# Performance work log

Hardware: AMD Instinct MI355X
Metric: run time of the kernel (lower is better)

Reference implementation:

```python
import jax, jax.numpy as jnp
import numpy as np

B, S, D, H, OUT = 64, 512, 128, 2, 8
TD, VD, AD = 300, 35, 74
DH = D // H
EPS = 1e-5


def _layernorm(x, g, b):
    m = jnp.mean(x, -1, keepdims=True)
    v = jnp.var(x, -1, keepdims=True)
    return (x - m) * jax.lax.rsqrt(v + EPS) * g + b


def _attn_neg(q_in, k_in, v_in, Wq, bq, Wk, bk, Wv, bv, Wd, bd, g, beta):
    # MultiheadAttention2: probs = 1 - softmax(scores). dropout off (eval).
    b_, s_, _ = q_in.shape
    q = (q_in @ Wq + bq).reshape(b_, s_, H, DH).transpose(0, 2, 1, 3)
    k = (k_in @ Wk + bk).reshape(b_, k_in.shape[1], H, DH).transpose(0, 2, 1, 3)
    v = (v_in @ Wv + bv).reshape(b_, v_in.shape[1], H, DH).transpose(0, 2, 1, 3)
    scores = jnp.einsum('bhqd,bhkd->bhqk', q, k) / jnp.sqrt(jnp.float32(DH))
    probs = 1.0 - jax.nn.softmax(scores, axis=-1)
    ctx = jnp.einsum('bhqk,bhkd->bhqd', probs, v)
    ctx = ctx.transpose(0, 2, 1, 3).reshape(b_, s_, D)
    return _layernorm(ctx @ Wd + bd, g, beta)


def _gru_dir(x, Wih, Whh, bih, bhh):
    # torch GRU, gate order (r, z, n). x: [B,S,D] -> [B,S,H=128]
    gx = x @ Wih.T + bih  # [B,S,3H]
    gx_t = gx.transpose(1, 0, 2)  # [S,B,3H]

    def step(h, g_t):
        gh = h @ Whh.T + bhh
        xr, xz, xn = jnp.split(g_t, 3, -1)
        hr, hz, hn = jnp.split(gh, 3, -1)
        r = jax.nn.sigmoid(xr + hr)
        z = jax.nn.sigmoid(xz + hz)
        n = jnp.tanh(xn + r * hn)
        h_new = (1.0 - z) * n + z * h
        return h_new, h_new

    h0 = jnp.zeros((x.shape[0], D), x.dtype)
    _, hs = jax.lax.scan(step, h0, gx_t)
    return hs.transpose(1, 0, 2)


def _bigru(x, Wih, Whh, bih, bhh):
    fwd = _gru_dir(x, Wih[0], Whh[0], bih[0], bhh[0])
    bwd = _gru_dir(x[:, ::-1], Wih[1], Whh[1], bih[1], bhh[1])[:, ::-1]
    return jnp.concatenate([fwd, bwd], -1)


def setup_inputs() -> dict:
    key = jax.random.key(0)
    ks = iter(jax.random.split(key, 40))
    sc = 0.05

    def rn(shape, s=sc):
        return jax.random.normal(next(ks), shape, jnp.float32) * s

    inp = {
        'text_features': rn((B, S, TD), 1.0),
        'visual_features': rn((B, S, VD), 1.0),
        'audio_features': rn((B, S, AD), 1.0),
        'fc1W': rn((TD, D)), 'fc1b': rn((D,)),
        'fc2W': rn((VD, D)), 'fc2b': rn((D,)),
        'fc3W': rn((AD, D)), 'fc3b': rn((D,)),
        # 6 attention units: [ta_a, ta_b, tv_a, tv_b, va_a, va_b]
        'Wq': rn((6, D, D)), 'bq': rn((6, D)),
        'Wk': rn((6, D, D)), 'bk': rn((6, D)),
        'Wv': rn((6, D, D)), 'bv': rn((6, D)),
        'Wd': rn((6, D, D)), 'bd': rn((6, D)),
        'ln_g': jnp.ones((6, D), jnp.float32), 'ln_b': jnp.zeros((6, D), jnp.float32),
        # 3 bidirectional GRUs: [gru1(text), gru2(visual), gru3(audio)] x [fwd, bwd]
        'gWih': rn((3, 2, 3 * D, D)), 'gWhh': rn((3, 2, 3 * D, D)),
        'gbih': rn((3, 2, 3 * D)), 'gbhh': rn((3, 2, 3 * D)),
        # head: Linear(3D,2D) -> BN(eval) -> ReLU6 -> Linear(2D,out)
        'fW1': rn((3 * D, 2 * D)), 'fb1': rn((2 * D,)),
        'bn_g': jnp.ones((2 * D,), jnp.float32), 'bn_b': jnp.zeros((2 * D,), jnp.float32),
        'fW2': rn((2 * D, OUT)), 'fb2': rn((OUT,)),
    }
    return inp


def reference(text_features, visual_features, audio_features,
              fc1W, fc1b, fc2W, fc2b, fc3W, fc3b,
              Wq, bq, Wk, bk, Wv, bv, Wd, bd, ln_g, ln_b,
              gWih, gWhh, gbih, gbhh,
              fW1, fb1, bn_g, bn_b, fW2, fb2):
    t = text_features @ fc1W + fc1b
    v = visual_features @ fc2W + fc2b
    a = audio_features @ fc3W + fc3b

    def A(i, q, k, val):
        return _attn_neg(q, k, val, Wq[i], bq[i], Wk[i], bk[i], Wv[i], bv[i],
                         Wd[i], bd[i], ln_g[i], ln_b[i])

    # CrossAttention(a,b): b_out = a_attn(a,b,b); a_out = b_attn(b,a,a)
    audio_out1 = A(0, t, a, a)   # text_audio.a_attention
    text_out1 = A(1, a, t, t)    # text_audio.b_attention
    visual_out1 = A(2, t, v, v)  # text_visual.a_attention
    text_out2 = A(3, v, t, t)    # text_visual.b_attention
    audio_out2 = A(4, v, a, a)   # visual_audio.a_attention
    visual_out2 = A(5, a, v, v)  # visual_audio.b_attention

    text_out = (text_out1 + text_out2) / 2
    visual_out = (visual_out1 + visual_out2) / 2
    audio_out = (audio_out1 + audio_out2) / 2

    text_out = _bigru(text_out, gWih[0], gWhh[0], gbih[0], gbhh[0])
    visual_out = _bigru(visual_out, gWih[1], gWhh[1], gbih[1], gbhh[1])
    audio_out = _bigru(audio_out, gWih[2], gWhh[2], gbih[2], gbhh[2])

    out = jnp.concatenate([text_out, visual_out, audio_out], -1)  # [B,S,6D]
    out = jnp.mean((out[:, :, 3 * D:] + out[:, :, :3 * D]) / 2, axis=1)  # [B,3D]

    h = out @ fW1 + fb1
    # BatchNorm1d in eval with running stats (mean=0, var=1)
    h = h * jax.lax.rsqrt(jnp.float32(1.0 + EPS)) * bn_g + bn_b
    h = jnp.clip(h, 0.0, 6.0)  # ReLU6
    return h @ fW2 + fb2
```

## Files before the change

### kernel.cpp

```cpp
#include <hip/hip_runtime.h>
#include <hip/hip_bf16.h>

#define BB 64
#define SS 512
#define DD 128
#define NROW (BB * SS)
#define SZ ((size_t)NROW * DD)

#define LOG2E 1.4426950408889634f
#define QSCALE (0.125f * LOG2E)

typedef __attribute__((ext_vector_type(8))) short short8;
typedef __attribute__((ext_vector_type(4))) float f32x4;

#define WB_P1 0
#define WB_P2 40960
#define WB_P3 49152
#define WB_QKVD 61440
#define WB_WIH 454656
#define WB_WHH 749568
#define WB_TOTAL 1044480

__device__ __forceinline__ float frcp_(float x) { return __builtin_amdgcn_rcpf(x); }
__device__ __forceinline__ float fexp2_(float x) { return __builtin_amdgcn_exp2f(x); }
__device__ __forceinline__ float b2f(unsigned short u) {
  union { unsigned int i; float f; } x; x.i = ((unsigned int)u) << 16; return x.f;
}
__device__ __forceinline__ unsigned short f2b(float f) {
  __hip_bfloat16 b = __float2bfloat16(f);
  return *reinterpret_cast<unsigned short*>(&b);
}
__device__ __forceinline__ unsigned short f2b_trunc(float f) {
  union { float f; unsigned int i; } x; x.f = f; return (unsigned short)(x.i >> 16);
}

__global__ __launch_bounds__(256) void prep_kernel(
    const float* __restrict__ fc1W, const float* __restrict__ fc2W,
    const float* __restrict__ fc3W, const float* __restrict__ Wq,
    const float* __restrict__ Wk, const float* __restrict__ Wv,
    const float* __restrict__ Wd, const float* __restrict__ gWih,
    const float* __restrict__ gWhh, const float* __restrict__ gbih,
    const float* __restrict__ gbhh, const float* __restrict__ bq,
    unsigned short* __restrict__ WB, float* __restrict__ gbihs,
    float* __restrict__ bqs) {
  for (int idx = blockIdx.x * 256 + threadIdx.x; idx < WB_TOTAL;
       idx += gridDim.x * 256) {
    float v;
    if (idx < WB_P2) {
      int n = idx / 320, k = idx % 320;
      v = (k < 300) ? fc1W[k * 128 + n] : 0.f;
    } else if (idx < WB_P3) {
      int r = idx - WB_P2; int n = r >> 6, k = r & 63;
      v = (k < 35) ? fc2W[k * 128 + n] : 0.f;
    } else if (idx < WB_QKVD) {
      int r = idx - WB_P3; int n = r / 96, k = r % 96;
      v = (k < 74) ? fc3W[k * 128 + n] : 0.f;
    } else if (idx < WB_WIH) {
      int r = idx - WB_QKVD;
      int op = r / 98304; int r2 = r % 98304;
      int u = r2 >> 14; int r3 = r2 & 16383;
      int n = r3 >> 7, k = r3 & 127;
      const float* src = (op == 0) ? Wq : (op == 1) ? Wk : (op == 2) ? Wv : Wd;
      v = src[u * 16384 + k * 128 + n];
      if (op == 0) v *= QSCALE;
    } else if (idx < WB_WHH) {
      int r = idx - WB_WIH;
      int r3 = r % 49152;
      int gate = (r3 >> 7) >> 7;
      v = gWih[r] * (gate < 2 ? LOG2E : 2.f * LOG2E);
    } else {
      int r = idx - WB_WHH;
      int r3 = r % 49152;
      int gate = (r3 >> 7) >> 7;
      v = gWhh[r] * (gate < 2 ? LOG2E : 2.f * LOG2E);
    }
    WB[idx] = f2b(v);
  }
  for (int idx = blockIdx.x * 256 + threadIdx.x; idx < 6 * 384;
       idx += gridDim.x * 256) {
    int gate = (idx % 384) >> 7;
    float v = gbih[idx] + (gate < 2 ? gbhh[idx] : 0.f);
    gbihs[idx] = v * (gate < 2 ? LOG2E : 2.f * LOG2E);
  }
  for (int idx = blockIdx.x * 256 + threadIdx.x; idx < 6 * 128;
       idx += gridDim.x * 256) {
    bqs[idx] = bq[idx] * QSCALE;
  }
}

struct GArg {
  const void* A; const unsigned short* W; const float* bias; void* C;
  int Ka, Kp, abf, cbf, cs; float* vsum;
};
struct GArgs { GArg g[18]; };

__global__ __launch_bounds__(256) void gemm_b(GArgs args) {
  const GArg ga = args.g[blockIdx.z];
  const int ny = blockIdx.y;
  __shared__ unsigned short As[128 * 40];
  __shared__ unsigned short Ws[128 * 40];
  const int t = threadIdx.x;
  const int w = t >> 6, lane = t & 63, q = lane >> 4, lm = lane & 15;
  const int wm = w >> 1, wn = w & 1;
  const int m0 = blockIdx.x * 128;
  const int row = t >> 1, cb = (t & 1) * 16;
  f32x4 acc[4][4];
#pragma unroll
  for (int i = 0; i < 4; ++i)
#pragma unroll
    for (int j = 0; j < 4; ++j) acc[i][j] = (f32x4){0.f, 0.f, 0.f, 0.f};

  for (int kt = 0; kt < ga.Kp; kt += 32) {
    {
      const float* Ag = (const float*)ga.A + (size_t)(m0 + row) * ga.Ka + kt + cb;
      unsigned short tmp[16];
#pragma unroll
      for (int j = 0; j < 16; ++j) {
        int k = kt + cb + j;
        tmp[j] = (k < ga.Ka) ? f2b(Ag[j]) : 0;
      }
      *reinterpret_cast<short8*>(&As[row * 40 + cb]) =
          *reinterpret_cast<short8*>(&tmp[0]);
      *reinterpret_cast<short8*>(&As[row * 40 + cb + 8]) =
          *reinterpret_cast<short8*>(&tmp[8]);
    }
    {
      const unsigned short* Wg =
          ga.W + (size_t)(ny * 128 + row) * ga.Kp + kt + cb;
      short8 v0 = *reinterpret_cast<const short8*>(Wg);
      short8 v1 = *reinterpret_cast<const short8*>(Wg + 8);
      *reinterpret_cast<short8*>(&Ws[row * 40 + cb]) = v0;
      *reinterpret_cast<short8*>(&Ws[row * 40 + cb + 8]) = v1;
    }
    __syncthreads();
    short8 af[4], bfv[4];
#pragma unroll
    for (int mi = 0; mi < 4; ++mi)
      af[mi] = *reinterpret_cast<const short8*>(
          &As[(wm * 64 + mi * 16 + lm) * 40 + q * 8]);
#pragma unroll
    for (int ni = 0; ni < 4; ++ni)
      bfv[ni] = *reinterpret_cast<const short8*>(
          &Ws[(wn * 64 + ni * 16 + lm) * 40 + q * 8]);
#pragma unroll
    for (int mi = 0; mi < 4; ++mi)
#pragma unroll
      for (int ni = 0; ni < 4; ++ni)
        acc[mi][ni] = __builtin_amdgcn_mfma_f32_16x16x32_bf16(
            af[mi], bfv[ni], acc[mi][ni], 0, 0, 0);
    __syncthreads();
  }
#pragma unroll
  for (int ni = 0; ni < 4; ++ni) {
    const int colg = ny * 128 + wn * 64 + ni * 16 + lm;
    const float bv = ga.bias[colg];
#pragma unroll
    for (int mi = 0; mi < 4; ++mi) {
      const int rg = m0 + wm * 64 + mi * 16 + q * 4;
#pragma unroll
      for (int r = 0; r < 4; ++r) {
        float v = acc[mi][ni][r] + bv;
        if (ga.cbf)
          ((unsigned short*)ga.C)[(size_t)(rg + r) * ga.cs + colg] = f2b(v);
        else
          ((float*)ga.C)[(size_t)(rg + r) * ga.cs + colg] = v;
      }
    }
  }
  if (ga.vsum) {
    float* vp = ga.vsum + (size_t)(m0 >> 9) * 128;
#pragma unroll
    for (int ni = 0; ni < 4; ++ni) {
      const int colg = wn * 64 + ni * 16 + lm;
      float s = 16.f * ga.bias[colg];
#pragma unroll
      for (int mi = 0; mi < 4; ++mi)
#pragma unroll
        for (int r = 0; r < 4; ++r) s += acc[mi][ni][r];
      atomicAdd(&vp[colg], s);
    }
  }
}

#define CST 5120

__global__ __launch_bounds__(256) void gemm_k128(GArgs args) {
  const GArg ga = args.g[blockIdx.z];
  const int ny = blockIdx.y;
  __shared__ unsigned short As4[4 * CST];
  __shared__ unsigned short Ws4[4 * CST];
  const int t = threadIdx.x;
  const int w = t >> 6, lane = t & 63, q = lane >> 4, lm = lane & 15;
  const int wm = w >> 1, wn = w & 1;
  const int m0 = blockIdx.x * 128;

  const int srow = t >> 4, scol = (t & 15) * 8;
  const int sc = scol >> 5, soff = scol & 31;
  {
    const unsigned short* Ab =
        (const unsigned short*)ga.A + (size_t)(m0 + srow) * 128 + scol;
    const unsigned short* Wg =
        ga.W + (size_t)(ny * 128 + srow) * 128 + scol;
#pragma unroll
    for (int p = 0; p < 8; ++p) {
      short8 av = *reinterpret_cast<const short8*>(Ab + (size_t)p * 16 * 128);
      short8 wv = *reinterpret_cast<const short8*>(Wg + (size_t)p * 16 * 128);
      *reinterpret_cast<short8*>(&As4[sc * CST + (srow + p * 16) * 40 + soff]) = av;
      *reinterpret_cast<short8*>(&Ws4[sc * CST + (srow + p * 16) * 40 + soff]) = wv;
    }
  }
  __syncthreads();

  f32x4 acc[4][4];
#pragma unroll
  for (int i = 0; i < 4; ++i)
#pragma unroll
    for (int j = 0; j < 4; ++j) acc[i][j] = (f32x4){0.f, 0.f, 0.f, 0.f};

#pragma unroll
  for (int c = 0; c < 4; ++c) {
    short8 af[4], bfv[4];
#pragma unroll
    for (int mi = 0; mi < 4; ++mi)
      af[mi] = *reinterpret_cast<const short8*>(
          &As4[c * CST + (wm * 64 + mi * 16 + lm) * 40 + q * 8]);
#pragma unroll
    for (int ni = 0; ni < 4; ++ni)
      bfv[ni] = *reinterpret_cast<const short8*>(
          &Ws4[c * CST + (wn * 64 + ni * 16 + lm) * 40 + q * 8]);
#pragma unroll
    for (int mi = 0; mi < 4; ++mi)
#pragma unroll
      for (int ni = 0; ni < 4; ++ni)
        acc[mi][ni] = __builtin_amdgcn_mfma_f32_16x16x32_bf16(
            af[mi], bfv[ni], acc[mi][ni], 0, 0, 0);
  }

#pragma unroll
  for (int ni = 0; ni < 4; ++ni) {
    const int colg = ny * 128 + wn * 64 + ni * 16 + lm;
    const float bv = ga.bias[colg];
#pragma unroll
    for (int mi = 0; mi < 4; ++mi) {
      const int rg = m0 + wm * 64 + mi * 16 + q * 4;
#pragma unroll
      for (int r = 0; r < 4; ++r) {
        float v = acc[mi][ni][r] + bv;
        if (ga.cbf)
          ((unsigned short*)ga.C)[(size_t)(rg + r) * ga.cs + colg] = f2b(v);
        else
          ((float*)ga.C)[(size_t)(rg + r) * ga.cs + colg] = v;
      }
    }
  }
  if (ga.vsum) {
    float* vp = ga.vsum + (size_t)(m0 >> 9) * 128;
#pragma unroll
    for (int ni = 0; ni < 4; ++ni) {
      const int colg = wn * 64 + ni * 16 + lm;
      float s = 16.f * ga.bias[colg];
#pragma unroll
      for (int mi = 0; mi < 4; ++mi)
#pragma unroll
        for (int r = 0; r < 4; ++r) s += acc[mi][ni][r];
      atomicAdd(&vp[colg], s);
    }
  }
}

__global__ __launch_bounds__(256) void attn2(
    const unsigned short* __restrict__ QKV, const float* __restrict__ VS,
    unsigned short* __restrict__ CTX) {
  __shared__ unsigned short Vt[64 * 72];
  __shared__ unsigned short Pt[4][16 * 72];
  const int t = threadIdx.x;
  const int w = t >> 6, lane = t & 63, quad = lane >> 4, lm = lane & 15;
  const int z = blockIdx.z;
  const int bh = blockIdx.y, b = bh >> 1, h = bh & 1;
  const int qbase = blockIdx.x * 256;

  const unsigned short* Qg = QKV + (size_t)(z * 3 + 0) * SZ;
  const unsigned short* Kg = QKV + (size_t)(z * 3 + 1) * SZ;
  const unsigned short* Vg = QKV + (size_t)(z * 3 + 2) * SZ;

  short8 aq[4][2];
#pragma unroll
  for (int qt = 0; qt < 4; ++qt)
#pragma unroll
    for (int c = 0; c < 2; ++c)
      aq[qt][c] = *reinterpret_cast<const short8*>(
          Qg + ((size_t)(b * SS + qbase + qt * 64 + w * 16 + lm)) * DD +
          h * 64 + c * 32 + quad * 8);

  const f32x4 czero = {0.f, 0.f, 0.f, 0.f};
  f32x4 o[4][4];
#pragma unroll
  for (int i = 0; i < 4; ++i)
#pragma unroll
    for (int j = 0; j < 4; ++j) o[i][j] = czero;
  float suml[4][4];
#pragma unroll
  for (int i = 0; i < 4; ++i)
#pragma unroll
    for (int j = 0; j < 4; ++j) suml[i][j] = 0.f;

  const int vk = t >> 3, vd0 = (t & 7) * 8;

  for (int kt = 0; kt < 8; ++kt) {
    const int k0 = kt * 64;
    __syncthreads();
#pragma unroll
    for (int i = 0; i < 2; ++i) {
      const int k = vk + i * 32;
      short8 vv = *reinterpret_cast<const short8*>(
          Vg + ((size_t)(b * SS + k0 + k)) * DD + h * 64 + vd0);
#pragma unroll
      for (int j = 0; j < 8; ++j) {
        const int d = vd0 + j;
        Vt[d * 72 + (k ^ (d & 56))] = (unsigned short)vv[j];
      }
    }
    __syncthreads();

    short8 bk[4][2];
#pragma unroll
    for (int nt = 0; nt < 4; ++nt)
#pragma unroll
      for (int c = 0; c < 2; ++c)
        bk[nt][c] = *reinterpret_cast<const short8*>(
            Kg + ((size_t)(b * SS + k0 + nt * 16 + lm)) * DD + h * 64 +
            c * 32 + quad * 8);
    short8 bvv[4][2];
#pragma unroll
    for (int dt = 0; dt < 4; ++dt) {
      const int d = dt * 16 + lm;
#pragma unroll
      for (int c = 0; c < 2; ++c)
        bvv[dt][c] = *reinterpret_cast<const short8*>(
            &Vt[d * 72 + ((c * 32 + quad * 8) ^ (d & 56))]);
    }

#pragma unroll
    for (int qt = 0; qt < 4; ++qt) {
      f32x4 sacc[4];
#pragma unroll
      for (int nt = 0; nt < 4; ++nt)
        sacc[nt] = __builtin_amdgcn_mfma_f32_16x16x32_bf16(
            aq[qt][0], bk[nt][0], czero, 0, 0, 0);
#pragma unroll
      for (int nt = 0; nt < 4; ++nt)
        sacc[nt] = __builtin_amdgcn_mfma_f32_16x16x32_bf16(
            aq[qt][1], bk[nt][1], sacc[nt], 0, 0, 0);
#pragma unroll
      for (int nt = 0; nt < 4; ++nt) {
#pragma unroll
        for (int r = 0; r < 4; ++r) {
          float p = fexp2_(sacc[nt][r]);
          suml[qt][r] += p;
          Pt[w][(quad * 4 + r) * 72 + nt * 16 + lm] = f2b_trunc(p);
        }
      }
#pragma unroll
      for (int c = 0; c < 2; ++c) {
        short8 ap = *reinterpret_cast<const short8*>(
            &Pt[w][lm * 72 + c * 32 + quad * 8]);
#pragma unroll
        for (int dt = 0; dt < 4; ++dt)
          o[qt][dt] = __builtin_amdgcn_mfma_f32_16x16x32_bf16(
              ap, bvv[dt][c], o[qt][dt], 0, 0, 0);
      }
    }
  }
#pragma unroll
  for (int qt = 0; qt < 4; ++qt)
#pragma unroll
    for (int r = 0; r < 4; ++r) {
#pragma unroll
      for (int m = 1; m < 16; m <<= 1)
        suml[qt][r] += __shfl_xor(suml[qt][r], m);
    }
  const float* vsp = VS + (size_t)(z * BB + b) * DD + h * 64;
#pragma unroll
  for (int qt = 0; qt < 4; ++qt)
#pragma unroll
    for (int dt = 0; dt < 4; ++dt) {
      const int col = dt * 16 + lm;
      const float vs = vsp[col];
#pragma unroll
      for (int r = 0; r < 4; ++r) {
        const int row = qbase + qt * 64 + w * 16 + quad * 4 + r;
        CTX[(size_t)z * SZ + ((size_t)(b * SS + row)) * DD + h * 64 + col] =
            f2b(vs - o[qt][dt][r] * frcp_(suml[qt][r]));
      }
    }
}

__global__ __launch_bounds__(256) void ln_pair(
    const unsigned short* __restrict__ DOUT, const float* __restrict__ lng,
    const float* __restrict__ lnb, unsigned short* __restrict__ GRUIN) {
  const int g = blockIdx.y;
  const int row = blockIdx.x * 4 + (threadIdx.x >> 6);
  const int t = threadIdx.x & 63;
  const int u1t[3] = {1, 2, 0};
  const int u2t[3] = {3, 5, 4};
  float outA = 0.f, outB = 0.f;
#pragma unroll
  for (int half = 0; half < 2; ++half) {
    const int u = half == 0 ? u1t[g] : u2t[g];
    const unsigned short* x = DOUT + (size_t)u * SZ + (size_t)row * DD;
    unsigned int xv = *reinterpret_cast<const unsigned int*>(x + 2 * t);
    float a = b2f((unsigned short)(xv & 0xffffu));
    float c = b2f((unsigned short)(xv >> 16));
    float s = a + c, sq = a * a + c * c;
#pragma unroll
    for (int off = 32; off > 0; off >>= 1) {
      s += __shfl_down(s, off);
      sq += __shfl_down(sq, off);
    }
    s = __shfl(s, 0); sq = __shfl(sq, 0);
    float mean = s * (1.f / 128.f);
    float var = sq * (1.f / 128.f) - mean * mean;
    float rs = rsqrtf(var + 1e-5f);
    const float* gg = lng + u * 128;
    const float* bb = lnb + u * 128;
    outA += (a - mean) * rs * gg[2 * t] + bb[2 * t];
    outB += (c - mean) * rs * gg[2 * t + 1] + bb[2 * t + 1];
  }
  unsigned short* op = GRUIN + (size_t)g * SZ + (size_t)row * DD;
  unsigned int pk = (unsigned int)f2b(0.5f * outA) |
                    ((unsigned int)f2b(0.5f * outB) << 16);
  *reinterpret_cast<unsigned int*>(op + 2 * t) = pk;
}

#define AST 136

__global__ __launch_bounds__(512, 1) void gru8(
    const unsigned short* __restrict__ GXR, const unsigned short* __restrict__ WB,
    const float* __restrict__ gbhh, float* __restrict__ HS) {
  __shared__ unsigned short Abuf[2][16 * AST];
  const int rec = blockIdx.y, bg = blockIdx.x;
  const int dir = rec & 1;
  const int t = threadIdx.x;
  const int w = t >> 6, lane = t & 63, q = lane >> 4, lm = lane & 15;
  const int o = w * 16 + lm;
  const int b = bg * 4 + q;

  short8 Bh[3][4];
  const unsigned short* whh = WB + WB_WHH + (size_t)rec * 49152;
#pragma unroll
  for (int gate = 0; gate < 3; ++gate)
#pragma unroll
    for (int c = 0; c < 4; ++c)
      Bh[gate][c] = *reinterpret_cast<const short8*>(
          whh + (size_t)(gate * 128 + o) * 128 + c * 32 + q * 8);
  const float bhn = gbhh[rec * 384 + 256 + o] * (2.f * LOG2E);
  const f32x4 czero = {0.f, 0.f, 0.f, 0.f};
  const f32x4 cbhn = {bhn, 0.f, 0.f, 0.f};

  float h = 0.f, hsum = 0.f;
  for (int i = t; i < 2 * 16 * AST; i += 512)
    (&Abuf[0][0])[i] = 0;

  const unsigned short* gx0 = GXR + (size_t)rec * 12582912 +
      ((size_t)b * 512 + (dir ? 511 : 0)) * 384 + o;
  const ptrdiff_t st = dir ? -384 : 384;

  unsigned short ring[4][3];
#pragma unroll
  for (int pp = 0; pp < 4; ++pp) {
    const unsigned short* gp = gx0 + (ptrdiff_t)pp * st;
#pragma unroll
    for (int j = 0; j < 3; ++j) ring[pp][j] = gp[j * 128];
  }
  const unsigned short* pf = gx0 + (ptrdiff_t)4 * st;
  __syncthreads();

#pragma unroll 4
  for (int s = 0; s < SS; ++s) {
    const int p = s & 1, slot = s & 3;
    const float gxr = b2f(ring[slot][0]);
    const float gxz = b2f(ring[slot][1]);
    const float gxn = b2f(ring[slot][2]);
#pragma unroll
    for (int j = 0; j < 3; ++j) ring[slot][j] = pf[j * 128];
    pf += (s < SS - 5) ? st : 0;

    short8 ah0 = *reinterpret_cast<const short8*>(&Abuf[p][lm * AST + 0 + q * 8]);
    short8 ah1 = *reinterpret_cast<const short8*>(&Abuf[p][lm * AST + 32 + q * 8]);
    short8 ah2 = *reinterpret_cast<const short8*>(&Abuf[p][lm * AST + 64 + q * 8]);
    short8 ah3 = *reinterpret_cast<const short8*>(&Abuf[p][lm * AST + 96 + q * 8]);
    f32x4 r0 = __builtin_amdgcn_mfma_f32_16x16x32_bf16(ah0, Bh[0][0], czero, 0, 0, 0);
    f32x4 r1 = __builtin_amdgcn_mfma_f32_16x16x32_bf16(ah2, Bh[0][2], czero, 0, 0, 0);
    f32x4 z0 = __builtin_amdgcn_mfma_f32_16x16x32_bf16(ah0, Bh[1][0], czero, 0, 0, 0);
    f32x4 z1 = __builtin_amdgcn_mfma_f32_16x16x32_bf16(ah2, Bh[1][2], czero, 0, 0, 0);
    f32x4 n0 = __builtin_amdgcn_mfma_f32_16x16x32_bf16(ah0, Bh[2][0], cbhn, 0, 0, 0);
    f32x4 n1 = __builtin_amdgcn_mfma_f32_16x16x32_bf16(ah2, Bh[2][2], czero, 0, 0, 0);
    r0 = __builtin_amdgcn_mfma_f32_16x16x32_bf16(ah1, Bh[0][1], r0, 0, 0, 0);
    r1 = __builtin_amdgcn_mfma_f32_16x16x32_bf16(ah3, Bh[0][3], r1, 0, 0, 0);
    z0 = __builtin_amdgcn_mfma_f32_16x16x32_bf16(ah1, Bh[1][1], z0, 0, 0, 0);
    z1 = __builtin_amdgcn_mfma_f32_16x16x32_bf16(ah3, Bh[1][3], z1, 0, 0, 0);
    n0 = __builtin_amdgcn_mfma_f32_16x16x32_bf16(ah1, Bh[2][1], n0, 0, 0, 0);
    n1 = __builtin_amdgcn_mfma_f32_16x16x32_bf16(ah3, Bh[2][3], n1, 0, 0, 0);

    float rr = frcp_(1.f + fexp2_(-(gxr + r0[0] + r1[0])));
    float zz = frcp_(1.f + fexp2_(-(gxz + z0[0] + z1[0])));
    float nn = 1.f - 2.f * frcp_(fexp2_(gxn + rr * (n0[0] + n1[0])) + 1.f);
    h = nn + zz * (h - nn);
    hsum += h;
    Abuf[p ^ 1][(q * 4) * AST + o] = f2b_trunc(h);
    asm volatile("s_waitcnt lgkmcnt(0)\n\ts_barrier" ::: "memory");
  }
  HS[((size_t)rec * BB + bg * 4 + q) * 128 + o] = hsum;
}

__global__ __launch_bounds__(256) void head_kernel(
    const float* __restrict__ HS, const float* __restrict__ fW1,
    const float* __restrict__ fb1, const float* __restrict__ bng,
    const float* __restrict__ bnb, const float* __restrict__ fW2,
    const float* __restrict__ fb2, float* __restrict__ out) {
  __shared__ float pl[384];
  __shared__ float h1[256];
  int b = blockIdx.x, n = threadIdx.x;
  {
    int j = n;
    int seg = j >> 7, oo = j & 127;
    pl[j] = (HS[((size_t)seg * BB + b) * 128 + oo] +
             HS[((size_t)(seg + 3) * BB + b) * 128 + oo]) * (0.5f / 512.f);
  }
  if (n < 128) {
    int j = 256 + n;
    int seg = j >> 7, oo = j & 127;
    pl[j] = (HS[((size_t)seg * BB + b) * 128 + oo] +
             HS[((size_t)(seg + 3) * BB + b) * 128 + oo]) * (0.5f / 512.f);
  }
  __syncthreads();
  float acc = fb1[n];
  for (int k = 0; k < 384; ++k) acc += pl[k] * fW1[k * 256 + n];
  float hv = acc * rsqrtf(1.f + 1e-5f) * bng[n] + bnb[n];
  hv = fminf(fmaxf(hv, 0.f), 6.f);
  h1[n] = hv;
  __syncthreads();
  if (n < 8) {
    float a2 = fb2[n];
    for (int k = 0; k < 256; ++k) a2 += h1[k] * fW2[k * 8 + n];
    out[b * 8 + n] = a2;
  }
}

extern "C" void kernel_launch(void* const* d_in, const int* in_sizes, int n_in,
                              void* d_out, int out_size, void* d_ws,
                              size_t ws_size, hipStream_t stream) {
  (void)in_sizes; (void)n_in; (void)out_size; (void)ws_size;
  const float* text = (const float*)d_in[0];
  const float* vis  = (const float*)d_in[1];
  const float* aud  = (const float*)d_in[2];
  const float* fc1W = (const float*)d_in[3];
  const float* fc1b = (const float*)d_in[4];
  const float* fc2W = (const float*)d_in[5];
  const float* fc2b = (const float*)d_in[6];
  const float* fc3W = (const float*)d_in[7];
  const float* fc3b = (const float*)d_in[8];
  const float* Wq = (const float*)d_in[9];
  const float* bq = (const float*)d_in[10];
  const float* Wk = (const float*)d_in[11];
  const float* bk = (const float*)d_in[12];
  const float* Wv = (const float*)d_in[13];
  const float* bv = (const float*)d_in[14];
  const float* Wd = (const float*)d_in[15];
  const float* bd = (const float*)d_in[16];
  const float* lng = (const float*)d_in[17];
  const float* lnb = (const float*)d_in[18];
  const float* gWih = (const float*)d_in[19];
  const float* gWhh = (const float*)d_in[20];
  const float* gbih = (const float*)d_in[21];
  const float* gbhh = (const float*)d_in[22];
  const float* fW1 = (const float*)d_in[23];
  const float* fb1 = (const float*)d_in[24];
  const float* bng = (const float*)d_in[25];
  const float* bnb = (const float*)d_in[26];
  const float* fW2 = (const float*)d_in[27];
  const float* fb2 = (const float*)d_in[28];
  float* out = (float*)d_out;

  unsigned short* WSB = (unsigned short*)d_ws;
  unsigned short* T   = WSB;
  unsigned short* Vv  = WSB + SZ;
  unsigned short* Aa  = WSB + 2 * SZ;
  unsigned short* QKV = WSB + 3 * SZ;
  unsigned short* CTX = WSB + 12 * SZ;
  unsigned short* DOUT = WSB;
  unsigned short* GXR = WSB;
  unsigned short* GRUIN = WSB + 18 * SZ;
  unsigned short* WB  = WSB + 21 * SZ;
  float* VS = (float*)(WSB + 21 * SZ + 1048576);
  float* HS = VS + 6 * 64 * 128;
  float* gbihs = HS + 6 * 64 * 128;
  float* bqs = gbihs + 6 * 384;

  prep_kernel<<<dim3(1024), dim3(256), 0, stream>>>(
      fc1W, fc2W, fc3W, Wq, Wk, Wv, Wd, gWih, gWhh, gbih, gbhh, bq, WB,
      gbihs, bqs);
  hipMemsetAsync(VS, 0, 6 * 64 * 128 * sizeof(float), stream);

  {
    GArgs ga{};
    ga.g[0] = {text, WB + WB_P1, fc1b, T, 300, 320, 0, 1, 128};
    ga.g[1] = {vis,  WB + WB_P2, fc2b, Vv, 35, 64, 0, 1, 128};
    ga.g[2] = {aud,  WB + WB_P3, fc3b, Aa, 74, 96, 0, 1, 128};
    gemm_b<<<dim3(256, 1, 3), dim3(256), 0, stream>>>(ga);
  }

  const int qsel[6] = {0, 2, 0, 1, 1, 2};
  const int ksel[6] = {2, 0, 1, 0, 2, 1};
  unsigned short* proj[3] = {T, Vv, Aa};

  for (int phase = 0; phase < 2; ++phase) {
    GArgs ga{};
    for (int ul = 0; ul < 3; ++ul) {
      int u = phase * 3 + ul;
      for (int op = 0; op < 3; ++op) {
        int z = ul * 3 + op;
        const float* bias = (op == 0) ? (bqs + u * 128)
                          : (op == 1) ? (bk + u * 128) : (bv + u * 128);
        float* vsum = (op == 2) ? (VS + (size_t)(phase * 3 + ul) * BB * DD)
                                : nullptr;
        ga.g[z] = {proj[op == 0 ? qsel[u] : ksel[u]],
                   WB + WB_QKVD + op * 98304 + u * 16384, bias,
                   QKV + (size_t)z * SZ, 128, 128, 1, 1, 128, vsum};
      }
    }
    gemm_k128<<<dim3(256, 1, 9), dim3(256), 0, stream>>>(ga);
    attn2<<<dim3(2, 128, 3), dim3(256), 0, stream>>>(
        QKV, VS + phase * 3 * BB * DD, CTX + (size_t)phase * 3 * SZ);
  }

  {
    GArgs ga{};
    for (int u = 0; u < 6; ++u)
      ga.g[u] = {CTX + (size_t)u * SZ, WB + WB_QKVD + 3 * 98304 + u * 16384,
                 bd + u * 128, DOUT + (size_t)u * SZ, 128, 128, 1, 1, 128};
    gemm_k128<<<dim3(256, 1, 6), dim3(256), 0, stream>>>(ga);
  }

  ln_pair<<<dim3(NROW / 4, 3), dim3(256), 0, stream>>>(DOUT, lng, lnb, GRUIN);

  {
    GArgs ga{};
    for (int r6 = 0; r6 < 6; ++r6) {
      int g = r6 >> 1;
      ga.g[r6] = {GRUIN + (size_t)g * SZ, WB + WB_WIH + r6 * 49152,
                  gbihs + r6 * 384, GXR + (size_t)r6 * 12582912,
                  128, 128, 1, 1, 384};
    }
    gemm_k128<<<dim3(256, 3, 6), dim3(256), 0, stream>>>(ga);
  }

  gru8<<<dim3(16, 6), dim3(512), 0, stream>>>(GXR, WB, gbhh, HS);
  head_kernel<<<dim3(BB), dim3(256), 0, stream>>>(HS, fW1, fb1, bng, bnb, fW2, fb2, out);
}
```

Before: 733.3 us.

## Group GEMMs sharing an A tile so each block reuses it across weights

Replaces the per-GEMM kernel with a grouped variant: each block loads its 128x128 A tile into shared memory once, then loops over several weight matrices that share that input, computing and storing each output in turn. Used for the QKV projections (grouped by source modality) and the GRU input projections (six weight slices per modality). This cuts redundant global reads of activations but lowers grid parallelism (fewer blocks, serial work per block) and adds a barrier per weight.

```diff
diff --git a/kernel.cpp b/kernel.cpp
--- a/kernel.cpp
+++ b/kernel.cpp
@@ -92,7 +92,7 @@
   const void* A; const unsigned short* W; const float* bias; void* C;
   int Ka, Kp, abf, cbf, cs; float* vsum;
 };
-struct GArgs { GArg g[18]; };
+struct GArgs { GArg g[18]; int gw; int pad_; };
 
 __global__ __launch_bounds__(256) void gemm_b(GArgs args) {
   const GArg ga = args.g[blockIdx.z];
@@ -184,86 +184,93 @@
 
 #define CST 5120
 
-__global__ __launch_bounds__(256) void gemm_k128(GArgs args) {
-  const GArg ga = args.g[blockIdx.z];
-  const int ny = blockIdx.y;
+__global__ __launch_bounds__(256) void gemm_k128g(GArgs args) {
+  const int base = blockIdx.z * args.gw;
+  const int nw = args.g[base].abf;
   __shared__ unsigned short As4[4 * CST];
   __shared__ unsigned short Ws4[4 * CST];
   const int t = threadIdx.x;
-  const int w = t >> 6, lane = t & 63, q = lane >> 4, lm = lane & 15;
-  const int wm = w >> 1, wn = w & 1;
+  const int lane = t & 63, q = lane >> 4, lm = lane & 15;
+  const int w = t >> 6, wm = w >> 1, wn = w & 1;
   const int m0 = blockIdx.x * 128;
 
   const int srow = t >> 4, scol = (t & 15) * 8;
   const int sc = scol >> 5, soff = scol & 31;
+
   {
     const unsigned short* Ab =
-        (const unsigned short*)ga.A + (size_t)(m0 + srow) * 128 + scol;
-    const unsigned short* Wg =
-        ga.W + (size_t)(ny * 128 + srow) * 128 + scol;
+        (const unsigned short*)args.g[base].A + (size_t)(m0 + srow) * 128 + scol;
 #pragma unroll
     for (int p = 0; p < 8; ++p) {
       short8 av = *reinterpret_cast<const short8*>(Ab + (size_t)p * 16 * 128);
-      short8 wv = *reinterpret_cast<const short8*>(Wg + (size_t)p * 16 * 128);
       *reinterpret_cast<short8*>(&As4[sc * CST + (srow + p * 16) * 40 + soff]) = av;
-      *reinterpret_cast<short8*>(&Ws4[sc * CST + (srow + p * 16) * 40 + soff]) = wv;
-    }
-  }
-  __syncthreads();
-
-  f32x4 acc[4][4];
-#pragma unroll
-  for (int i = 0; i < 4; ++i)
-#pragma unroll
-    for (int j = 0; j < 4; ++j) acc[i][j] = (f32x4){0.f, 0.f, 0.f, 0.f};
-
-#pragma unroll
-  for (int c = 0; c < 4; ++c) {
-    short8 af[4], bfv[4];
-#pragma unroll
-    for (int mi = 0; mi < 4; ++mi)
-      af[mi] = *reinterpret_cast<const short8*>(
-          &As4[c * CST + (wm * 64 + mi * 16 + lm) * 40 + q * 8]);
-#pragma unroll
-    for (int ni = 0; ni < 4; ++ni)
-      bfv[ni] = *reinterpret_cast<const short8*>(
-          &Ws4[c * CST + (wn * 64 + ni * 16 + lm) * 40 + q * 8]);
-#pragma unroll
-    for (int mi = 0; mi < 4; ++mi)
+    }
+  }
+
+  for (int i = 0; i < nw; ++i) {
+    const GArg ge = args.g[base + i];
+    if (i) __syncthreads();
+    {
+      const unsigned short* Wg = ge.W + (size_t)srow * 128 + scol;
+#pragma unroll
+      for (int p = 0; p < 8; ++p) {
+        short8 wv = *reinterpret_cast<const short8*>(Wg + (size_t)p * 16 * 128);
+        *reinterpret_cast<short8*>(&Ws4[sc * CST + (srow + p * 16) * 40 + soff]) = wv;
+      }
+    }
+    __syncthreads();
+
+    f32x4 acc[4][4];
+#pragma unroll
+    for (int ii = 0; ii < 4; ++ii)
+#pragma unroll
+      for (int jj = 0; jj < 4; ++jj) acc[ii][jj] = (f32x4){0.f, 0.f, 0.f, 0.f};
+
+#pragma unroll
+    for (int c = 0; c < 4; ++c) {
+      short8 af[4], bfv[4];
+#pragma unroll
+      for (int mi = 0; mi < 4; ++mi)
+        af[mi] = *reinterpret_cast<const short8*>(
+            &As4[c * CST + (wm * 64 + mi * 16 + lm) * 40 + q * 8]);
 #pragma unroll
       for (int ni = 0; ni < 4; ++ni)
-        acc[mi][ni] = __builtin_amdgcn_mfma_f32_16x16x32_bf16(
-            af[mi], bfv[ni], acc[mi][ni], 0, 0, 0);
-  }
-
-#pragma unroll
-  for (int ni = 0; ni < 4; ++ni) {
-    const int colg = ny * 128 + wn * 64 + ni * 16 + lm;
-    const float bv = ga.bias[colg];
-#pragma unroll
-    for (int mi = 0; mi < 4; ++mi) {
-      const int rg = m0 + wm * 64 + mi * 16 + q * 4;
-#pragma unroll
-      for (int r = 0; r < 4; ++r) {
-        float v = acc[mi][ni][r] + bv;
-        if (ga.cbf)
-          ((unsigned short*)ga.C)[(size_t)(rg + r) * ga.cs + colg] = f2b(v);
-        else
-          ((float*)ga.C)[(size_t)(rg + r) * ga.cs + colg] = v;
-      }
-    }
-  }
-  if (ga.vsum) {
-    float* vp = ga.vsum + (size_t)(m0 >> 9) * 128;
+        bfv[ni] = *reinterpret_cast<const short8*>(
+            &Ws4[c * CST + (wn * 64 + ni * 16 + lm) * 40 + q * 8]);
+#pragma unroll
+      for (int mi = 0; mi < 4; ++mi)
+#pragma unroll
+        for (int ni = 0; ni < 4; ++ni)
+          acc[mi][ni] = __builtin_amdgcn_mfma_f32_16x16x32_bf16(
+              af[mi], bfv[ni], acc[mi][ni], 0, 0, 0);
+    }
+
 #pragma unroll
     for (int ni = 0; ni < 4; ++ni) {
       const int colg = wn * 64 + ni * 16 + lm;
-      float s = 16.f * ga.bias[colg];
-#pragma unroll
-      for (int mi = 0; mi < 4; ++mi)
-#pragma unroll
-        for (int r = 0; r < 4; ++r) s += acc[mi][ni][r];
-      atomicAdd(&vp[colg], s);
+      const float bv = ge.bias[colg];
+#pragma unroll
+      for (int mi = 0; mi < 4; ++mi) {
+        const int rg = m0 + wm * 64 + mi * 16 + q * 4;
+#pragma unroll
+        for (int r = 0; r < 4; ++r) {
+          float v = acc[mi][ni][r] + bv;
+          ((unsigned short*)ge.C)[(size_t)(rg + r) * ge.cs + colg] = f2b(v);
+        }
+      }
+    }
+    if (ge.vsum) {
+      float* vp = ge.vsum + (size_t)(m0 >> 9) * 128;
+#pragma unroll
+      for (int ni = 0; ni < 4; ++ni) {
+        const int colg = wn * 64 + ni * 16 + lm;
+        float s = 16.f * ge.bias[colg];
+#pragma unroll
+        for (int mi = 0; mi < 4; ++mi)
+#pragma unroll
+          for (int r = 0; r < 4; ++r) s += acc[mi][ni][r];
+        atomicAdd(&vp[colg], s);
+      }
     }
   }
 }
@@ -616,43 +623,54 @@
 
   for (int phase = 0; phase < 2; ++phase) {
     GArgs ga{};
+    ga.gw = 4;
+    int cnt[3] = {0, 0, 0};
     for (int ul = 0; ul < 3; ++ul) {
       int u = phase * 3 + ul;
       for (int op = 0; op < 3; ++op) {
+        int a = (op == 0) ? qsel[u] : ksel[u];
         int z = ul * 3 + op;
         const float* bias = (op == 0) ? (bqs + u * 128)
                           : (op == 1) ? (bk + u * 128) : (bv + u * 128);
-        float* vsum = (op == 2) ? (VS + (size_t)(phase * 3 + ul) * BB * DD)
-                                : nullptr;
-        ga.g[z] = {proj[op == 0 ? qsel[u] : ksel[u]],
-                   WB + WB_QKVD + op * 98304 + u * 16384, bias,
-                   QKV + (size_t)z * SZ, 128, 128, 1, 1, 128, vsum};
-      }
-    }
-    gemm_k128<<<dim3(256, 1, 9), dim3(256), 0, stream>>>(ga);
+        float* vsum = (op == 2) ? (VS + (size_t)u * BB * DD) : nullptr;
+        ga.g[a * 4 + cnt[a]] = {proj[a],
+                                WB + WB_QKVD + op * 98304 + u * 16384, bias,
+                                QKV + (size_t)z * SZ, 128, 128, 0, 1, 128,
+                                vsum};
+        cnt[a]++;
+      }
+    }
+    for (int a = 0; a < 3; ++a) ga.g[a * 4].abf = cnt[a];
+    gemm_k128g<<<dim3(256, 1, 3), dim3(256), 0, stream>>>(ga);
     attn2<<<dim3(2, 128, 3), dim3(256), 0, stream>>>(
         QKV, VS + phase * 3 * BB * DD, CTX + (size_t)phase * 3 * SZ);
   }
 
   {
     GArgs ga{};
+    ga.gw = 1;
     for (int u = 0; u < 6; ++u)
       ga.g[u] = {CTX + (size_t)u * SZ, WB + WB_QKVD + 3 * 98304 + u * 16384,
                  bd + u * 128, DOUT + (size_t)u * SZ, 128, 128, 1, 1, 128};
-    gemm_k128<<<dim3(256, 1, 6), dim3(256), 0, stream>>>(ga);
+    gemm_k128g<<<dim3(256, 1, 6), dim3(256), 0, stream>>>(ga);
   }
 
   ln_pair<<<dim3(NROW / 4, 3), dim3(256), 0, stream>>>(DOUT, lng, lnb, GRUIN);
 
   {
     GArgs ga{};
-    for (int r6 = 0; r6 < 6; ++r6) {
-      int g = r6 >> 1;
-      ga.g[r6] = {GRUIN + (size_t)g * SZ, WB + WB_WIH + r6 * 49152,
-                  gbihs + r6 * 384, GXR + (size_t)r6 * 12582912,
-                  128, 128, 1, 1, 384};
-    }
-    gemm_k128<<<dim3(256, 3, 6), dim3(256), 0, stream>>>(ga);
+    ga.gw = 6;
+    for (int g = 0; g < 3; ++g) {
+      for (int i = 0; i < 6; ++i) {
+        int dr = i / 3, ny = i % 3, r6 = g * 2 + dr;
+        ga.g[g * 6 + i] = {GRUIN + (size_t)g * SZ,
+                           WB + WB_WIH + r6 * 49152 + ny * 16384,
+                           gbihs + r6 * 384 + ny * 128,
+                           GXR + (size_t)r6 * 12582912 + ny * 128,
+                           128, 128, (i == 0) ? 6 : 0, 1, 384, nullptr};
+      }
+    }
+    gemm_k128g<<<dim3(256, 1, 3), dim3(256), 0, stream>>>(ga);
   }
 
   gru8<<<dim3(16, 6), dim3(512), 0, stream>>>(GXR, WB, gbhh, HS);
```

New measurement: 710.2 us. 1.03x faster.
